# Kernel optimization log

Hardware: AMD Instinct MI355X
Metric: run time of the kernel (lower is better)

Reference implementation:

```python
import jax, jax.numpy as jnp
import numpy as np

B, T, D, K = 8, 2048, 384, 64

def setup_inputs() -> dict:
    key = jax.random.key(0)
    k1, k2, k3, k4 = jax.random.split(key, 4)
    x = jax.random.normal(k1, (B, T, D), dtype=jnp.float32)
    # torch nn.Linear default init scale ~ 1/sqrt(fan_in); use scaled normals
    Wq = jax.random.normal(k2, (D, K), dtype=jnp.float32) / np.sqrt(D)
    Wk = jax.random.normal(k3, (D, K), dtype=jnp.float32) / np.sqrt(D)
    Wv = jax.random.normal(k4, (D, D), dtype=jnp.float32) / np.sqrt(D)
    return {"x": x, "Wq": Wq, "Wk": Wk, "Wv": Wv}

def reference(x, Wq, Wk, Wv):
    # x: (B,T,D)
    q = jnp.einsum('btd,dk->btk', x, Wq)      # (B,T,K)
    k = jnp.einsum('btd,dk->btk', x, Wk)      # (B,T,K)
    v = jnp.einsum('btd,de->bte', x, Wv)      # (B,T,D)
    scores = jnp.einsum('bqk,bsk->bqs', q, k) / jnp.sqrt(jnp.float32(K))  # (B,T,T)
    causal = jnp.tril(jnp.ones((T, T), dtype=bool))
    scores = jnp.where(causal, scores, -jnp.inf)
    weights = jax.nn.softmax(scores, axis=-1)
    out = jnp.einsum('bqs,bse->bqe', weights, v)  # (B,T,D)
    return out
```

## Files before the change

### kernel.cpp

```cpp
#include <hip/hip_runtime.h>

#define TT 2048
#define DD 384

typedef float f32x4 __attribute__((ext_vector_type(4)));
typedef float f32x16 __attribute__((ext_vector_type(16)));
typedef short s16x8 __attribute__((ext_vector_type(8)));
typedef short s16x2 __attribute__((ext_vector_type(2)));
typedef unsigned int u32x4 __attribute__((ext_vector_type(4)));
typedef unsigned int u32x2 __attribute__((ext_vector_type(2)));

typedef __attribute__((address_space(3))) unsigned char* as3p;
typedef const __attribute__((address_space(1))) unsigned char* as1p;
#define GLLDS(gsrc, ldst) __builtin_amdgcn_global_load_lds((as1p)(gsrc), (as3p)(ldst), 16, 0, 0)

static __device__ __forceinline__ unsigned short f2bf(float f) {
    unsigned int u = __builtin_bit_cast(unsigned int, f);
    u = (u + 0x7fffu + ((u >> 16) & 1u)) >> 16;
    return (unsigned short)u;
}
static __device__ __forceinline__ unsigned int pk2(float a, float b) {
#if __has_builtin(__builtin_amdgcn_cvt_pk_bf16_f32)
    s16x2 t = __builtin_amdgcn_cvt_pk_bf16_f32(a, b);
    return __builtin_bit_cast(unsigned int, t);
#else
    unsigned int ua = __builtin_bit_cast(unsigned int, a);
    unsigned int ub = __builtin_bit_cast(unsigned int, b);
    ua = (ua + 0x7fffu + ((ua >> 16) & 1u)) >> 16;
    ub = (ub + 0x7fffu + ((ub >> 16) & 1u)) & 0xffff0000u;
    return ua | ub;
#endif
}

__global__ __launch_bounds__(256, 2) void qkv_gemm(
    const float* __restrict__ x, const float* __restrict__ Wq,
    const float* __restrict__ Wk, const float* __restrict__ Wv,
    unsigned short* __restrict__ qo, unsigned short* __restrict__ ko,
    unsigned short* __restrict__ vto)
{
    __shared__ __align__(16) unsigned short lds[16384];
    const int tid = threadIdx.x;
    const int l   = tid & 63;
    const int w   = tid >> 6;
    const int si  = l & 15;
    const int qq  = l >> 4;
    const int m0  = blockIdx.x * 128;
    const int nb  = blockIdx.y;
    const int wr  = w >> 1, wc = w & 1;

    const int bn = tid & 127;
    const int bk = (tid >> 7) * 16;
    const float* wsrc; int ldw;
    if (nb == 0) { wsrc = (bn < 64) ? (Wq + bn) : (Wk + (bn - 64)); ldw = 64; }
    else         { wsrc = Wv + (nb - 1) * 128 + bn;                 ldw = 384; }

    f32x4 acc[4][4];
    #pragma unroll
    for (int rt = 0; rt < 4; ++rt)
        #pragma unroll
        for (int ct = 0; ct < 4; ++ct) acc[rt][ct] = (f32x4){0.f, 0.f, 0.f, 0.f};

    for (int kt = 0; kt < 12; ++kt) {
        const int k0 = kt * 32;
        #pragma unroll
        for (int i = 0; i < 2; ++i) {
            const int u = tid + 256 * i, r = u >> 2, c = u & 3;
            const float* xp = x + (size_t)(m0 + r) * DD + k0 + c * 8;
            f32x4 x0 = *(const f32x4*)xp;
            f32x4 x1 = *(const f32x4*)(xp + 4);
            u32x4 av = (u32x4){pk2(x0[0], x0[1]), pk2(x0[2], x0[3]),
                               pk2(x1[0], x1[1]), pk2(x1[2], x1[3])};
            *(s16x8*)&lds[r * 32 + ((c ^ (r & 3)) * 8)] = __builtin_bit_cast(s16x8, av);
        }
        {
            float t[16];
            #pragma unroll
            for (int j = 0; j < 16; ++j) t[j] = wsrc[(size_t)(k0 + bk + j) * ldw];
            #pragma unroll
            for (int jj = 0; jj < 2; ++jj) {
                u32x4 bv = (u32x4){pk2(t[jj * 8 + 0], t[jj * 8 + 1]), pk2(t[jj * 8 + 2], t[jj * 8 + 3]),
                                   pk2(t[jj * 8 + 4], t[jj * 8 + 5]), pk2(t[jj * 8 + 6], t[jj * 8 + 7])};
                const int ch = (tid >> 7) * 2 + jj;
                *(s16x8*)&lds[4096 + bn * 32 + ((ch ^ (bn & 3)) * 8)] = __builtin_bit_cast(s16x8, bv);
            }
        }
        __syncthreads();

        s16x8 af[4], bf[4];
        #pragma unroll
        for (int rt = 0; rt < 4; ++rt) {
            const int row = wr * 64 + rt * 16 + si;
            af[rt] = *(const s16x8*)&lds[row * 32 + ((qq ^ (row & 3)) * 8)];
        }
        #pragma unroll
        for (int ct = 0; ct < 4; ++ct) {
            const int col = wc * 64 + ct * 16 + si;
            bf[ct] = *(const s16x8*)&lds[4096 + col * 32 + ((qq ^ (col & 3)) * 8)];
        }
        #pragma unroll
        for (int rt = 0; rt < 4; ++rt)
            #pragma unroll
            for (int ct = 0; ct < 4; ++ct)
                acc[rt][ct] = __builtin_amdgcn_mfma_f32_16x16x32_bf16(af[rt], bf[ct], acc[rt][ct], 0, 0, 0);
        __syncthreads();
    }

    if (nb == 0) {
        if (wc == 0) {
            #pragma unroll
            for (int rt = 0; rt < 4; ++rt)
                #pragma unroll
                for (int ct = 0; ct < 4; ++ct)
                    #pragma unroll
                    for (int r = 0; r < 4; ++r) {
                        const int m = m0 + wr * 64 + rt * 16 + qq * 4 + r;
                        qo[(size_t)m * 64 + ct * 16 + si] = f2bf(acc[rt][ct][r] * 0.125f);
                    }
        } else {
            #pragma unroll
            for (int rt = 0; rt < 4; ++rt)
                #pragma unroll
                for (int ct = 0; ct < 4; ++ct)
                    #pragma unroll
                    for (int r = 0; r < 4; ++r) {
                        const int m = m0 + wr * 64 + rt * 16 + qq * 4 + r;
                        const int col = ct * 16 + si;
                        ko[(size_t)m * 64 + (((col >> 3) ^ (m & 7)) * 8) + (col & 7)] = f2bf(acc[rt][ct][r]);
                    }
        }
    } else {
        #pragma unroll
        for (int rt = 0; rt < 4; ++rt)
            #pragma unroll
            for (int ct = 0; ct < 4; ++ct)
                #pragma unroll
                for (int r = 0; r < 4; ++r) {
                    const int m = wr * 64 + rt * 16 + qq * 4 + r;
                    const int n = wc * 64 + ct * 16 + si;
                    lds[n * 128 + (((m >> 3) ^ (n & 7)) * 8) + (m & 7)] = f2bf(acc[rt][ct][r]);
                }
        __syncthreads();
        const int bbat = m0 >> 11, t0 = m0 & 2047;
        #pragma unroll
        for (int i = 0; i < 8; ++i) {
            const int u = tid + 256 * i, n = u >> 4, mc = u & 15;
            s16x8 v = *(const s16x8*)&lds[n * 128 + ((mc ^ (n & 7)) * 8)];
            *(s16x8*)&vto[((size_t)bbat * DD + ((nb - 1) * 128 + n)) * TT
                          + t0 + (mc >> 3) * 64 + (((mc & 7) ^ (n & 7)) * 8)] = v;
        }
    }
}

__global__ __launch_bounds__(768, 3) void attn(
    const unsigned short* __restrict__ qg, const unsigned short* __restrict__ kg,
    const unsigned short* __restrict__ vg, float* __restrict__ out)
{
    __shared__ __align__(16) unsigned short lds[53248];

    const int tid = threadIdx.x;
    const int l   = tid & 63;
    const int w   = tid >> 6;
    const int qh  = w & 1;
    const int eu  = w >> 1;
    const bool isprod = (w < 4);
    const int lo  = l & 31;
    const int hi  = l >> 5;

    const int g  = blockIdx.x;
    const int bb = g & 7;
    const int eh = (g >> 3) & 1;
    const int pr = g >> 4;
    const int e0 = eh * 192;

    const unsigned short* kbase = kg + (size_t)bb * TT * 64;
    const unsigned short* vbase = vg + ((size_t)bb * DD + e0) * TT;

    #define STAGE(IT, KB, VB)                                                              \
    {                                                                                      \
        if (isprod) {                                                                      \
            GLLDS(kbase + (size_t)(IT) * 4096 + (2 * w) * 512 + l * 8,                     \
                  &lds[(KB) * 4096 + (2 * w) * 512]);                                      \
            GLLDS(kbase + (size_t)(IT) * 4096 + (2 * w + 1) * 512 + l * 8,                 \
                  &lds[(KB) * 4096 + (2 * w + 1) * 512]);                                  \
        } else {                                                                           \
            _Pragma("unroll")                                                              \
            for (int c3 = 0; c3 < 3; ++c3) {                                               \
                const int rg = 3 * (w - 4) + c3;                                           \
                GLLDS(vbase + (size_t)(rg * 8 + (l >> 3)) * TT + (IT) * 64 + (l & 7) * 8,  \
                      &lds[8192 + (VB) * 12288 + rg * 512]);                               \
            }                                                                              \
        }                                                                                  \
    }

    #define PVSTEP(VB, PB)                                                                 \
    {                                                                                      \
        __builtin_amdgcn_s_setprio(1);                                                     \
        _Pragma("unroll")                                                                  \
        for (int ss = 0; ss < 2; ++ss) {                                                   \
            const int pbse = 45056 + (PB) * 4096 + (qh * 2 + ss) * 1024;                   \
            s16x8 a0 = *(const s16x8*)&lds[pbse + l * 8];                                  \
            s16x8 a1 = *(const s16x8*)&lds[pbse + 512 + l * 8];                            \
            const int el = eu * 32 + lo;                                                   \
            const int vbse = 8192 + (VB) * 12288 + el * 64;                                \
            s16x8 v0 = *(const s16x8*)&lds[vbse + (((ss * 4 + hi) ^ (el & 7)) * 8)];       \
            o = __builtin_amdgcn_mfma_f32_32x32x16_bf16(a0, v0, o, 0, 0, 0);               \
            s16x8 v1 = *(const s16x8*)&lds[vbse + (((ss * 4 + 2 + hi) ^ (el & 7)) * 8)];   \
            o = __builtin_amdgcn_mfma_f32_32x32x16_bf16(a1, v1, o, 0, 0, 0);               \
        }                                                                                  \
        __builtin_amdgcn_s_setprio(0);                                                     \
    }

    for (int hf = 0; hf < 2; ++hf) {
        const int q2 = hf ? pr : 31 - pr;
        const int q0 = q2 * 64;
        const int qrow = q0 + qh * 32 + lo;

        s16x8 qf[4];
        if (isprod) {
            const unsigned short* qp = qg + ((size_t)bb * TT + qrow) * 64;
            #pragma unroll
            for (int st = 0; st < 4; ++st) qf[st] = *(const s16x8*)(qp + st * 16 + hi * 8);
        }

        f32x16 o;
        #pragma unroll
        for (int r = 0; r < 16; ++r) o[r] = 0.f;
        float lp = 0.f;

        STAGE(0, 0, 0);

        int vi = 0, vn = 1;
        for (int it = 0; it <= q2; ++it) {
            const int kb = it & 1;
            __syncthreads();

            if (it < q2) STAGE(it + 1, 1 - kb, vn);

            if (isprod) {
                f32x16 sa;
                #pragma unroll
                for (int r = 0; r < 16; ++r) sa[r] = 0.f;
                __builtin_amdgcn_s_setprio(1);
                #pragma unroll
                for (int st = 0; st < 4; ++st) {
                    s16x8 kf = *(const s16x8*)&lds[kb * 4096 + (eu * 32 + lo) * 64 + (((st * 2 + hi) ^ (lo & 7)) * 8)];
                    sa = __builtin_amdgcn_mfma_f32_32x32x16_bf16(kf, qf[st], sa, 0, 0, 0);
                }
                __builtin_amdgcn_s_setprio(0);
                const bool mb = (it == q2);
                float pv[16];
                #pragma unroll
                for (int r = 0; r < 16; ++r) {
                    float e = __expf(sa[r]);
                    if (mb) {
                        const int srow = it * 64 + eu * 32 + (r & 3) + 8 * (r >> 2) + 4 * hi;
                        if (srow > qrow) e = 0.f;
                    }
                    pv[r] = e;
                    lp += e;
                }
                unsigned int d0 = pk2(pv[0], pv[1]),   d1 = pk2(pv[2], pv[3]);
                unsigned int d2 = pk2(pv[4], pv[5]),   d3 = pk2(pv[6], pv[7]);
                unsigned int d4 = pk2(pv[8], pv[9]),   d5 = pk2(pv[10], pv[11]);
                unsigned int d6 = pk2(pv[12], pv[13]), d7 = pk2(pv[14], pv[15]);
                u32x4 fa0, fa1;
#if __has_builtin(__builtin_amdgcn_permlane32_swap)
                {
                    u32x2 s02 = __builtin_bit_cast(u32x2, __builtin_amdgcn_permlane32_swap(d0, d2, false, false));
                    u32x2 s13 = __builtin_bit_cast(u32x2, __builtin_amdgcn_permlane32_swap(d1, d3, false, false));
                    u32x2 s46 = __builtin_bit_cast(u32x2, __builtin_amdgcn_permlane32_swap(d4, d6, false, false));
                    u32x2 s57 = __builtin_bit_cast(u32x2, __builtin_amdgcn_permlane32_swap(d5, d7, false, false));
                    fa0 = (u32x4){s02[0], s13[0], s02[1], s13[1]};
                    fa1 = (u32x4){s46[0], s57[0], s46[1], s57[1]};
                }
#else
                {
                    unsigned int sA0 = hi ? d0 : d2, sA1 = hi ? d1 : d3;
                    unsigned int rA0 = (unsigned int)__shfl_xor((int)sA0, 32);
                    unsigned int rA1 = (unsigned int)__shfl_xor((int)sA1, 32);
                    fa0 = hi ? (u32x4){rA0, rA1, d2, d3} : (u32x4){d0, d1, rA0, rA1};
                    unsigned int sB0 = hi ? d4 : d6, sB1 = hi ? d5 : d7;
                    unsigned int rB0 = (unsigned int)__shfl_xor((int)sB0, 32);
                    unsigned int rB1 = (unsigned int)__shfl_xor((int)sB1, 32);
                    fa1 = hi ? (u32x4){rB0, rB1, d6, d7} : (u32x4){d4, d5, rB0, rB1};
                }
#endif
                *(s16x8*)&lds[45056 + kb * 4096 + (qh * 2 + eu) * 1024 + l * 8]       = __builtin_bit_cast(s16x8, fa0);
                *(s16x8*)&lds[45056 + kb * 4096 + (qh * 2 + eu) * 1024 + 512 + l * 8] = __builtin_bit_cast(s16x8, fa1);
            }

            if (it > 0) {
                const int vp = (vi == 0) ? 2 : vi - 1;
                PVSTEP(vp, 1 - kb);
            }

            vi = vn; vn = (vn == 2) ? 0 : vn + 1;
        }
        __syncthreads();
        {
            const int vlast = (vi == 0) ? 2 : vi - 1;
            PVSTEP(vlast, q2 & 1);
        }
        if (isprod) {
            float lt = lp + __shfl_xor(lp, 32);
            if (hi == 0) ((float*)lds)[(qh * 2 + eu) * 32 + lo] = lt;
        }
        __syncthreads();

        {
            const float* stL = (const float*)lds;
            #pragma unroll
            for (int r = 0; r < 16; ++r) {
                const int rloc = (r & 3) + 8 * (r >> 2) + 4 * hi;
                const float linv = 1.f / (stL[(qh * 2) * 32 + rloc] + stL[(qh * 2 + 1) * 32 + rloc]);
                out[((size_t)bb * TT + q0 + qh * 32 + rloc) * DD + e0 + eu * 32 + lo]
                    = o[r] * linv;
            }
        }
        __syncthreads();
    }
    #undef STAGE
    #undef PVSTEP
}

extern "C" void kernel_launch(void* const* d_in, const int* in_sizes, int n_in,
                              void* d_out, int out_size, void* d_ws, size_t ws_size,
                              hipStream_t stream)
{
    const float* x  = (const float*)d_in[0];
    const float* Wq = (const float*)d_in[1];
    const float* Wk = (const float*)d_in[2];
    const float* Wv = (const float*)d_in[3];

    unsigned short* qws  = (unsigned short*)d_ws;
    unsigned short* kws  = (unsigned short*)((char*)d_ws + ((size_t)2 << 20));
    unsigned short* vtws = (unsigned short*)((char*)d_ws + ((size_t)4 << 20));

    qkv_gemm<<<dim3(128, 4), dim3(256), 0, stream>>>(x, Wq, Wk, Wv, qws, kws, vtws);
    attn<<<dim3(256), dim3(768), 0, stream>>>(qws, kws, vtws, (float*)d_out);
}
```

Before: 133.4 us.

## Restructure attention to per-32-row query blocks with full-width value tiles

The attention kernel now assigns one 32-row query tile to each block, with 2 producer waves computing QK^T/exp and 6 consumer waves each covering 64 value columns over the full 384 width. This replaces the old scheme of 64-row tiles split into two 192-wide column halves and processed as paired heavy/light halves. V fragments are register double-buffered, each K tile's exp is computed once for all value columns, and blocks launch in descending work order. The QKV GEMM loops over two column blocks per workgroup, halving its grid. In exchange, the attention grid has more blocks with fewer threads each and uses more LDS and registers per block.

```diff
diff --git a/kernel.cpp b/kernel.cpp
--- a/kernel.cpp
+++ b/kernel.cpp
@@ -45,282 +45,300 @@
     const int si  = l & 15;
     const int qq  = l >> 4;
     const int m0  = blockIdx.x * 128;
-    const int nb  = blockIdx.y;
+    const int nbp = blockIdx.y;
     const int wr  = w >> 1, wc = w & 1;
 
     const int bn = tid & 127;
     const int bk = (tid >> 7) * 16;
-    const float* wsrc; int ldw;
-    if (nb == 0) { wsrc = (bn < 64) ? (Wq + bn) : (Wk + (bn - 64)); ldw = 64; }
-    else         { wsrc = Wv + (nb - 1) * 128 + bn;                 ldw = 384; }
-
-    f32x4 acc[4][4];
-    #pragma unroll
-    for (int rt = 0; rt < 4; ++rt)
-        #pragma unroll
-        for (int ct = 0; ct < 4; ++ct) acc[rt][ct] = (f32x4){0.f, 0.f, 0.f, 0.f};
-
-    for (int kt = 0; kt < 12; ++kt) {
-        const int k0 = kt * 32;
-        #pragma unroll
-        for (int i = 0; i < 2; ++i) {
-            const int u = tid + 256 * i, r = u >> 2, c = u & 3;
-            const float* xp = x + (size_t)(m0 + r) * DD + k0 + c * 8;
-            f32x4 x0 = *(const f32x4*)xp;
-            f32x4 x1 = *(const f32x4*)(xp + 4);
-            u32x4 av = (u32x4){pk2(x0[0], x0[1]), pk2(x0[2], x0[3]),
-                               pk2(x1[0], x1[1]), pk2(x1[2], x1[3])};
-            *(s16x8*)&lds[r * 32 + ((c ^ (r & 3)) * 8)] = __builtin_bit_cast(s16x8, av);
-        }
-        {
-            float t[16];
-            #pragma unroll
-            for (int j = 0; j < 16; ++j) t[j] = wsrc[(size_t)(k0 + bk + j) * ldw];
-            #pragma unroll
-            for (int jj = 0; jj < 2; ++jj) {
-                u32x4 bv = (u32x4){pk2(t[jj * 8 + 0], t[jj * 8 + 1]), pk2(t[jj * 8 + 2], t[jj * 8 + 3]),
-                                   pk2(t[jj * 8 + 4], t[jj * 8 + 5]), pk2(t[jj * 8 + 6], t[jj * 8 + 7])};
-                const int ch = (tid >> 7) * 2 + jj;
-                *(s16x8*)&lds[4096 + bn * 32 + ((ch ^ (bn & 3)) * 8)] = __builtin_bit_cast(s16x8, bv);
-            }
-        }
-        __syncthreads();
-
-        s16x8 af[4], bf[4];
-        #pragma unroll
-        for (int rt = 0; rt < 4; ++rt) {
-            const int row = wr * 64 + rt * 16 + si;
-            af[rt] = *(const s16x8*)&lds[row * 32 + ((qq ^ (row & 3)) * 8)];
-        }
-        #pragma unroll
-        for (int ct = 0; ct < 4; ++ct) {
-            const int col = wc * 64 + ct * 16 + si;
-            bf[ct] = *(const s16x8*)&lds[4096 + col * 32 + ((qq ^ (col & 3)) * 8)];
-        }
+
+    for (int nbi = 0; nbi < 2; ++nbi) {
+        const int nb = nbp * 2 + nbi;
+        const float* wsrc; int ldw;
+        if (nb == 0) { wsrc = (bn < 64) ? (Wq + bn) : (Wk + (bn - 64)); ldw = 64; }
+        else         { wsrc = Wv + (nb - 1) * 128 + bn;                 ldw = 384; }
+
+        f32x4 acc[4][4];
         #pragma unroll
         for (int rt = 0; rt < 4; ++rt)
             #pragma unroll
-            for (int ct = 0; ct < 4; ++ct)
-                acc[rt][ct] = __builtin_amdgcn_mfma_f32_16x16x32_bf16(af[rt], bf[ct], acc[rt][ct], 0, 0, 0);
-        __syncthreads();
-    }
-
-    if (nb == 0) {
-        if (wc == 0) {
+            for (int ct = 0; ct < 4; ++ct) acc[rt][ct] = (f32x4){0.f, 0.f, 0.f, 0.f};
+
+        for (int kt = 0; kt < 12; ++kt) {
+            const int k0 = kt * 32;
+            #pragma unroll
+            for (int i = 0; i < 2; ++i) {
+                const int u = tid + 256 * i, r = u >> 2, c = u & 3;
+                const float* xp = x + (size_t)(m0 + r) * DD + k0 + c * 8;
+                f32x4 x0 = *(const f32x4*)xp;
+                f32x4 x1 = *(const f32x4*)(xp + 4);
+                u32x4 av = (u32x4){pk2(x0[0], x0[1]), pk2(x0[2], x0[3]),
+                                   pk2(x1[0], x1[1]), pk2(x1[2], x1[3])};
+                *(s16x8*)&lds[r * 32 + ((c ^ (r & 3)) * 8)] = __builtin_bit_cast(s16x8, av);
+            }
+            {
+                float t[16];
+                #pragma unroll
+                for (int j = 0; j < 16; ++j) t[j] = wsrc[(size_t)(k0 + bk + j) * ldw];
+                #pragma unroll
+                for (int jj = 0; jj < 2; ++jj) {
+                    u32x4 bv = (u32x4){pk2(t[jj * 8 + 0], t[jj * 8 + 1]), pk2(t[jj * 8 + 2], t[jj * 8 + 3]),
+                                       pk2(t[jj * 8 + 4], t[jj * 8 + 5]), pk2(t[jj * 8 + 6], t[jj * 8 + 7])};
+                    const int ch = (tid >> 7) * 2 + jj;
+                    *(s16x8*)&lds[4096 + bn * 32 + ((ch ^ (bn & 3)) * 8)] = __builtin_bit_cast(s16x8, bv);
+                }
+            }
+            __syncthreads();
+
+            s16x8 af[4], bf[4];
+            #pragma unroll
+            for (int rt = 0; rt < 4; ++rt) {
+                const int row = wr * 64 + rt * 16 + si;
+                af[rt] = *(const s16x8*)&lds[row * 32 + ((qq ^ (row & 3)) * 8)];
+            }
+            #pragma unroll
+            for (int ct = 0; ct < 4; ++ct) {
+                const int col = wc * 64 + ct * 16 + si;
+                bf[ct] = *(const s16x8*)&lds[4096 + col * 32 + ((qq ^ (col & 3)) * 8)];
+            }
+            #pragma unroll
+            for (int rt = 0; rt < 4; ++rt)
+                #pragma unroll
+                for (int ct = 0; ct < 4; ++ct)
+                    acc[rt][ct] = __builtin_amdgcn_mfma_f32_16x16x32_bf16(af[rt], bf[ct], acc[rt][ct], 0, 0, 0);
+            __syncthreads();
+        }
+
+        if (nb == 0) {
+            if (wc == 0) {
+                #pragma unroll
+                for (int rt = 0; rt < 4; ++rt)
+                    #pragma unroll
+                    for (int ct = 0; ct < 4; ++ct)
+                        #pragma unroll
+                        for (int r = 0; r < 4; ++r) {
+                            const int m = m0 + wr * 64 + rt * 16 + qq * 4 + r;
+                            qo[(size_t)m * 64 + ct * 16 + si] = f2bf(acc[rt][ct][r] * 0.125f);
+                        }
+            } else {
+                #pragma unroll
+                for (int rt = 0; rt < 4; ++rt)
+                    #pragma unroll
+                    for (int ct = 0; ct < 4; ++ct)
+                        #pragma unroll
+                        for (int r = 0; r < 4; ++r) {
+                            const int m = m0 + wr * 64 + rt * 16 + qq * 4 + r;
+                            const int col = ct * 16 + si;
+                            ko[(size_t)m * 64 + (((col >> 3) ^ (m & 7)) * 8) + (col & 7)] = f2bf(acc[rt][ct][r]);
+                        }
+            }
+        } else {
             #pragma unroll
             for (int rt = 0; rt < 4; ++rt)
                 #pragma unroll
                 for (int ct = 0; ct < 4; ++ct)
                     #pragma unroll
                     for (int r = 0; r < 4; ++r) {
-                        const int m = m0 + wr * 64 + rt * 16 + qq * 4 + r;
-                        qo[(size_t)m * 64 + ct * 16 + si] = f2bf(acc[rt][ct][r] * 0.125f);
+                        const int m = wr * 64 + rt * 16 + qq * 4 + r;
+                        const int n = wc * 64 + ct * 16 + si;
+                        lds[n * 128 + (((m >> 3) ^ (n & 7)) * 8) + (m & 7)] = f2bf(acc[rt][ct][r]);
                     }
-        } else {
-            #pragma unroll
-            for (int rt = 0; rt < 4; ++rt)
-                #pragma unroll
-                for (int ct = 0; ct < 4; ++ct)
-                    #pragma unroll
-                    for (int r = 0; r < 4; ++r) {
-                        const int m = m0 + wr * 64 + rt * 16 + qq * 4 + r;
-                        const int col = ct * 16 + si;
-                        ko[(size_t)m * 64 + (((col >> 3) ^ (m & 7)) * 8) + (col & 7)] = f2bf(acc[rt][ct][r]);
-                    }
+            __syncthreads();
+            const int bbat = m0 >> 11, t0 = m0 & 2047;
+            #pragma unroll
+            for (int i = 0; i < 8; ++i) {
+                const int u = tid + 256 * i, n = u >> 4, mc = u & 15;
+                s16x8 v = *(const s16x8*)&lds[n * 128 + ((mc ^ (n & 7)) * 8)];
+                *(s16x8*)&vto[((size_t)bbat * DD + ((nb - 1) * 128 + n)) * TT
+                              + t0 + (mc >> 3) * 64 + (((mc & 7) ^ (n & 7)) * 8)] = v;
+            }
         }
-    } else {
-        #pragma unroll
-        for (int rt = 0; rt < 4; ++rt)
-            #pragma unroll
-            for (int ct = 0; ct < 4; ++ct)
-                #pragma unroll
-                for (int r = 0; r < 4; ++r) {
-                    const int m = wr * 64 + rt * 16 + qq * 4 + r;
-                    const int n = wc * 64 + ct * 16 + si;
-                    lds[n * 128 + (((m >> 3) ^ (n & 7)) * 8) + (m & 7)] = f2bf(acc[rt][ct][r]);
-                }
         __syncthreads();
-        const int bbat = m0 >> 11, t0 = m0 & 2047;
-        #pragma unroll
-        for (int i = 0; i < 8; ++i) {
-            const int u = tid + 256 * i, n = u >> 4, mc = u & 15;
-            s16x8 v = *(const s16x8*)&lds[n * 128 + ((mc ^ (n & 7)) * 8)];
-            *(s16x8*)&vto[((size_t)bbat * DD + ((nb - 1) * 128 + n)) * TT
-                          + t0 + (mc >> 3) * 64 + (((mc & 7) ^ (n & 7)) * 8)] = v;
-        }
-    }
-}
-
-__global__ __launch_bounds__(768, 3) void attn(
+    }
+}
+
+__global__ __launch_bounds__(512, 2) void attn(
     const unsigned short* __restrict__ qg, const unsigned short* __restrict__ kg,
     const unsigned short* __restrict__ vg, float* __restrict__ out)
 {
-    __shared__ __align__(16) unsigned short lds[53248];
+    __shared__ __align__(16) unsigned short lds[61440];
 
     const int tid = threadIdx.x;
     const int l   = tid & 63;
     const int w   = tid >> 6;
-    const int qh  = w & 1;
-    const int eu  = w >> 1;
-    const bool isprod = (w < 4);
+    const bool isprod = (w < 2);
+    const int cw  = w - 2;
     const int lo  = l & 31;
     const int hi  = l >> 5;
 
     const int g  = blockIdx.x;
     const int bb = g & 7;
-    const int eh = (g >> 3) & 1;
-    const int pr = g >> 4;
-    const int e0 = eh * 192;
+    const int q1 = 63 - (g >> 3);
+    const int q0 = q1 * 32;
+    const int itm = q1 >> 1;
+    const int qrow = q0 + lo;
+
+    s16x8 qf[4];
+    if (isprod) {
+        const unsigned short* qp = qg + ((size_t)bb * TT + qrow) * 64;
+        #pragma unroll
+        for (int st = 0; st < 4; ++st) qf[st] = *(const s16x8*)(qp + st * 16 + hi * 8);
+    }
+
+    f32x16 o[2];
+    #pragma unroll
+    for (int et = 0; et < 2; ++et)
+        #pragma unroll
+        for (int r = 0; r < 16; ++r) o[et][r] = 0.f;
+    float lp = 0.f;
+    s16x8 vfA[8], vfB[8];
 
     const unsigned short* kbase = kg + (size_t)bb * TT * 64;
-    const unsigned short* vbase = vg + ((size_t)bb * DD + e0) * TT;
-
-    #define STAGE(IT, KB, VB)                                                              \
+    const unsigned short* vbase = vg + (size_t)bb * DD * TT;
+
+    #define STAGE(IT, BUF)                                                                 \
     {                                                                                      \
         if (isprod) {                                                                      \
-            GLLDS(kbase + (size_t)(IT) * 4096 + (2 * w) * 512 + l * 8,                     \
-                  &lds[(KB) * 4096 + (2 * w) * 512]);                                      \
-            GLLDS(kbase + (size_t)(IT) * 4096 + (2 * w + 1) * 512 + l * 8,                 \
-                  &lds[(KB) * 4096 + (2 * w + 1) * 512]);                                  \
+            _Pragma("unroll")                                                              \
+            for (int c = 0; c < 4; ++c) {                                                  \
+                const int ch = w * 4 + c;                                                  \
+                GLLDS(kbase + (size_t)(IT) * 4096 + ch * 512 + l * 8,                      \
+                      &lds[(BUF) * 4096 + ch * 512]);                                      \
+            }                                                                              \
         } else {                                                                           \
             _Pragma("unroll")                                                              \
-            for (int c3 = 0; c3 < 3; ++c3) {                                               \
-                const int rg = 3 * (w - 4) + c3;                                           \
+            for (int c = 0; c < 8; ++c) {                                                  \
+                const int rg = cw * 8 + c;                                                 \
                 GLLDS(vbase + (size_t)(rg * 8 + (l >> 3)) * TT + (IT) * 64 + (l & 7) * 8,  \
-                      &lds[8192 + (VB) * 12288 + rg * 512]);                               \
+                      &lds[8192 + (BUF) * 24576 + rg * 512]);                              \
             }                                                                              \
         }                                                                                  \
     }
 
-    #define PVSTEP(VB, PB)                                                                 \
+    #define LOADV(VF, VB)                                                                  \
+    {                                                                                      \
+        _Pragma("unroll")                                                                  \
+        for (int ss = 0; ss < 2; ++ss)                                                     \
+            _Pragma("unroll")                                                              \
+            for (int et = 0; et < 2; ++et) {                                               \
+                const int el = cw * 64 + et * 32 + lo;                                     \
+                const int vbse = 8192 + (VB) * 24576 + el * 64;                            \
+                VF[ss * 4 + et * 2 + 0] = *(const s16x8*)&lds[vbse + (((ss * 4 + hi) ^ (el & 7)) * 8)];     \
+                VF[ss * 4 + et * 2 + 1] = *(const s16x8*)&lds[vbse + (((ss * 4 + 2 + hi) ^ (el & 7)) * 8)]; \
+            }                                                                              \
+    }
+
+    #define PVC(VF, PB)                                                                    \
     {                                                                                      \
         __builtin_amdgcn_s_setprio(1);                                                     \
         _Pragma("unroll")                                                                  \
         for (int ss = 0; ss < 2; ++ss) {                                                   \
-            const int pbse = 45056 + (PB) * 4096 + (qh * 2 + ss) * 1024;                   \
+            const int pbse = 57344 + (PB) * 2048 + ss * 1024;                              \
             s16x8 a0 = *(const s16x8*)&lds[pbse + l * 8];                                  \
             s16x8 a1 = *(const s16x8*)&lds[pbse + 512 + l * 8];                            \
-            const int el = eu * 32 + lo;                                                   \
-            const int vbse = 8192 + (VB) * 12288 + el * 64;                                \
-            s16x8 v0 = *(const s16x8*)&lds[vbse + (((ss * 4 + hi) ^ (el & 7)) * 8)];       \
-            o = __builtin_amdgcn_mfma_f32_32x32x16_bf16(a0, v0, o, 0, 0, 0);               \
-            s16x8 v1 = *(const s16x8*)&lds[vbse + (((ss * 4 + 2 + hi) ^ (el & 7)) * 8)];   \
-            o = __builtin_amdgcn_mfma_f32_32x32x16_bf16(a1, v1, o, 0, 0, 0);               \
+            _Pragma("unroll")                                                              \
+            for (int et = 0; et < 2; ++et) {                                               \
+                o[et] = __builtin_amdgcn_mfma_f32_32x32x16_bf16(a0, VF[ss * 4 + et * 2 + 0], o[et], 0, 0, 0); \
+                o[et] = __builtin_amdgcn_mfma_f32_32x32x16_bf16(a1, VF[ss * 4 + et * 2 + 1], o[et], 0, 0, 0); \
+            }                                                                              \
         }                                                                                  \
         __builtin_amdgcn_s_setprio(0);                                                     \
     }
 
-    for (int hf = 0; hf < 2; ++hf) {
-        const int q2 = hf ? pr : 31 - pr;
-        const int q0 = q2 * 64;
-        const int qrow = q0 + qh * 32 + lo;
-
-        s16x8 qf[4];
+    STAGE(0, 0);
+
+    for (int it = 0; it <= itm; ++it) {
+        const int kb = it & 1;
+        __syncthreads();
+
+        if (it < itm) STAGE(it + 1, 1 - kb);
+
         if (isprod) {
-            const unsigned short* qp = qg + ((size_t)bb * TT + qrow) * 64;
-            #pragma unroll
-            for (int st = 0; st < 4; ++st) qf[st] = *(const s16x8*)(qp + st * 16 + hi * 8);
+            f32x16 sa;
+            #pragma unroll
+            for (int r = 0; r < 16; ++r) sa[r] = 0.f;
+            __builtin_amdgcn_s_setprio(1);
+            #pragma unroll
+            for (int st = 0; st < 4; ++st) {
+                s16x8 kf = *(const s16x8*)&lds[kb * 4096 + (w * 32 + lo) * 64 + (((st * 2 + hi) ^ (lo & 7)) * 8)];
+                sa = __builtin_amdgcn_mfma_f32_32x32x16_bf16(kf, qf[st], sa, 0, 0, 0);
+            }
+            __builtin_amdgcn_s_setprio(0);
+            const bool mb = (it == itm);
+            float pv[16];
+            #pragma unroll
+            for (int r = 0; r < 16; ++r) {
+                float e = __expf(sa[r]);
+                if (mb) {
+                    const int srow = it * 64 + w * 32 + (r & 3) + 8 * (r >> 2) + 4 * hi;
+                    if (srow > qrow) e = 0.f;
+                }
+                pv[r] = e;
+                lp += e;
+            }
+            unsigned int d0 = pk2(pv[0], pv[1]),   d1 = pk2(pv[2], pv[3]);
+            unsigned int d2 = pk2(pv[4], pv[5]),   d3 = pk2(pv[6], pv[7]);
+            unsigned int d4 = pk2(pv[8], pv[9]),   d5 = pk2(pv[10], pv[11]);
+            unsigned int d6 = pk2(pv[12], pv[13]), d7 = pk2(pv[14], pv[15]);
+            u32x4 fa0, fa1;
+#if __has_builtin(__builtin_amdgcn_permlane32_swap)
+            {
+                u32x2 s02 = __builtin_bit_cast(u32x2, __builtin_amdgcn_permlane32_swap(d0, d2, false, false));
+                u32x2 s13 = __builtin_bit_cast(u32x2, __builtin_amdgcn_permlane32_swap(d1, d3, false, false));
+                u32x2 s46 = __builtin_bit_cast(u32x2, __builtin_amdgcn_permlane32_swap(d4, d6, false, false));
+                u32x2 s57 = __builtin_bit_cast(u32x2, __builtin_amdgcn_permlane32_swap(d5, d7, false, false));
+                fa0 = (u32x4){s02[0], s13[0], s02[1], s13[1]};
+                fa1 = (u32x4){s46[0], s57[0], s46[1], s57[1]};
+            }
+#else
+            {
+                unsigned int sA0 = hi ? d0 : d2, sA1 = hi ? d1 : d3;
+                unsigned int rA0 = (unsigned int)__shfl_xor((int)sA0, 32);
+                unsigned int rA1 = (unsigned int)__shfl_xor((int)sA1, 32);
+                fa0 = hi ? (u32x4){rA0, rA1, d2, d3} : (u32x4){d0, d1, rA0, rA1};
+                unsigned int sB0 = hi ? d4 : d6, sB1 = hi ? d5 : d7;
+                unsigned int rB0 = (unsigned int)__shfl_xor((int)sB0, 32);
+                unsigned int rB1 = (unsigned int)__shfl_xor((int)sB1, 32);
+                fa1 = hi ? (u32x4){rB0, rB1, d6, d7} : (u32x4){d4, d5, rB0, rB1};
+            }
+#endif
+            *(s16x8*)&lds[57344 + kb * 2048 + w * 1024 + l * 8]       = __builtin_bit_cast(s16x8, fa0);
+            *(s16x8*)&lds[57344 + kb * 2048 + w * 1024 + 512 + l * 8] = __builtin_bit_cast(s16x8, fa1);
+        } else {
+            if (it & 1) {
+                if (it > 0) PVC(vfA, 1 - kb);
+                LOADV(vfB, kb);
+            } else {
+                if (it > 0) PVC(vfB, 1 - kb);
+                LOADV(vfA, kb);
+            }
         }
-
-        f32x16 o;
+    }
+    __syncthreads();
+
+    if (isprod) {
+        float lt = lp + __shfl_xor(lp, 32);
+        if (hi == 0) ((float*)lds)[w * 32 + lo] = lt;
+    } else {
+        if (itm & 1) { PVC(vfB, itm & 1); }
+        else         { PVC(vfA, itm & 1); }
+    }
+    __syncthreads();
+
+    if (!isprod) {
+        const float* stL = (const float*)lds;
         #pragma unroll
-        for (int r = 0; r < 16; ++r) o[r] = 0.f;
-        float lp = 0.f;
-
-        STAGE(0, 0, 0);
-
-        int vi = 0, vn = 1;
-        for (int it = 0; it <= q2; ++it) {
-            const int kb = it & 1;
-            __syncthreads();
-
-            if (it < q2) STAGE(it + 1, 1 - kb, vn);
-
-            if (isprod) {
-                f32x16 sa;
-                #pragma unroll
-                for (int r = 0; r < 16; ++r) sa[r] = 0.f;
-                __builtin_amdgcn_s_setprio(1);
-                #pragma unroll
-                for (int st = 0; st < 4; ++st) {
-                    s16x8 kf = *(const s16x8*)&lds[kb * 4096 + (eu * 32 + lo) * 64 + (((st * 2 + hi) ^ (lo & 7)) * 8)];
-                    sa = __builtin_amdgcn_mfma_f32_32x32x16_bf16(kf, qf[st], sa, 0, 0, 0);
-                }
-                __builtin_amdgcn_s_setprio(0);
-                const bool mb = (it == q2);
-                float pv[16];
-                #pragma unroll
-                for (int r = 0; r < 16; ++r) {
-                    float e = __expf(sa[r]);
-                    if (mb) {
-                        const int srow = it * 64 + eu * 32 + (r & 3) + 8 * (r >> 2) + 4 * hi;
-                        if (srow > qrow) e = 0.f;
-                    }
-                    pv[r] = e;
-                    lp += e;
-                }
-                unsigned int d0 = pk2(pv[0], pv[1]),   d1 = pk2(pv[2], pv[3]);
-                unsigned int d2 = pk2(pv[4], pv[5]),   d3 = pk2(pv[6], pv[7]);
-                unsigned int d4 = pk2(pv[8], pv[9]),   d5 = pk2(pv[10], pv[11]);
-                unsigned int d6 = pk2(pv[12], pv[13]), d7 = pk2(pv[14], pv[15]);
-                u32x4 fa0, fa1;
-#if __has_builtin(__builtin_amdgcn_permlane32_swap)
-                {
-                    u32x2 s02 = __builtin_bit_cast(u32x2, __builtin_amdgcn_permlane32_swap(d0, d2, false, false));
-                    u32x2 s13 = __builtin_bit_cast(u32x2, __builtin_amdgcn_permlane32_swap(d1, d3, false, false));
-                    u32x2 s46 = __builtin_bit_cast(u32x2, __builtin_amdgcn_permlane32_swap(d4, d6, false, false));
-                    u32x2 s57 = __builtin_bit_cast(u32x2, __builtin_amdgcn_permlane32_swap(d5, d7, false, false));
-                    fa0 = (u32x4){s02[0], s13[0], s02[1], s13[1]};
-                    fa1 = (u32x4){s46[0], s57[0], s46[1], s57[1]};
-                }
-#else
-                {
-                    unsigned int sA0 = hi ? d0 : d2, sA1 = hi ? d1 : d3;
-                    unsigned int rA0 = (unsigned int)__shfl_xor((int)sA0, 32);
-                    unsigned int rA1 = (unsigned int)__shfl_xor((int)sA1, 32);
-                    fa0 = hi ? (u32x4){rA0, rA1, d2, d3} : (u32x4){d0, d1, rA0, rA1};
-                    unsigned int sB0 = hi ? d4 : d6, sB1 = hi ? d5 : d7;
-                    unsigned int rB0 = (unsigned int)__shfl_xor((int)sB0, 32);
-                    unsigned int rB1 = (unsigned int)__shfl_xor((int)sB1, 32);
-                    fa1 = hi ? (u32x4){rB0, rB1, d6, d7} : (u32x4){d4, d5, rB0, rB1};
-                }
-#endif
-                *(s16x8*)&lds[45056 + kb * 4096 + (qh * 2 + eu) * 1024 + l * 8]       = __builtin_bit_cast(s16x8, fa0);
-                *(s16x8*)&lds[45056 + kb * 4096 + (qh * 2 + eu) * 1024 + 512 + l * 8] = __builtin_bit_cast(s16x8, fa1);
-            }
-
-            if (it > 0) {
-                const int vp = (vi == 0) ? 2 : vi - 1;
-                PVSTEP(vp, 1 - kb);
-            }
-
-            vi = vn; vn = (vn == 2) ? 0 : vn + 1;
-        }
-        __syncthreads();
-        {
-            const int vlast = (vi == 0) ? 2 : vi - 1;
-            PVSTEP(vlast, q2 & 1);
-        }
-        if (isprod) {
-            float lt = lp + __shfl_xor(lp, 32);
-            if (hi == 0) ((float*)lds)[(qh * 2 + eu) * 32 + lo] = lt;
-        }
-        __syncthreads();
-
-        {
-            const float* stL = (const float*)lds;
+        for (int et = 0; et < 2; ++et)
             #pragma unroll
             for (int r = 0; r < 16; ++r) {
                 const int rloc = (r & 3) + 8 * (r >> 2) + 4 * hi;
-                const float linv = 1.f / (stL[(qh * 2) * 32 + rloc] + stL[(qh * 2 + 1) * 32 + rloc]);
-                out[((size_t)bb * TT + q0 + qh * 32 + rloc) * DD + e0 + eu * 32 + lo]
-                    = o[r] * linv;
-            }
-        }
-        __syncthreads();
+                const float linv = 1.f / (stL[rloc] + stL[32 + rloc]);
+                out[((size_t)bb * TT + q0 + rloc) * DD + cw * 64 + et * 32 + lo]
+                    = o[et][r] * linv;
+            }
     }
     #undef STAGE
-    #undef PVSTEP
+    #undef LOADV
+    #undef PVC
 }
 
 extern "C" void kernel_launch(void* const* d_in, const int* in_sizes, int n_in,
@@ -336,6 +354,6 @@
     unsigned short* kws  = (unsigned short*)((char*)d_ws + ((size_t)2 << 20));
     unsigned short* vtws = (unsigned short*)((char*)d_ws + ((size_t)4 << 20));
 
-    qkv_gemm<<<dim3(128, 4), dim3(256), 0, stream>>>(x, Wq, Wk, Wv, qws, kws, vtws);
-    attn<<<dim3(256), dim3(768), 0, stream>>>(qws, kws, vtws, (float*)d_out);
-}
+    qkv_gemm<<<dim3(128, 2), dim3(256), 0, stream>>>(x, Wq, Wk, Wv, qws, kws, vtws);
+    attn<<<dim3(512), dim3(512), 0, stream>>>(qws, kws, vtws, (float*)d_out);
+}
```

Result: slower. 176.6 us (+32.4%).

## Pre-pack weights to bf16 and double-buffer QKV GEMM with direct LDS loads

Applied to the files above, without the earlier changes.

A new small kernel converts Wq, Wk and Wv each call into one packed, pre-swizzled bf16 weight matrix in workspace. The QKV GEMM then streams weight tiles straight into LDS with global_load_lds and double-buffers the x and W stages, so the next tile loads while MFMAs run. The M tile is halved to 64 rows, which doubles the grid and raises the occupancy hint, and the V-transpose epilogue is simplified to match. The cost is an extra kernel launch and more workspace traffic in exchange for removing strided fp32 weight loads and conversions from the GEMM inner loop.

```diff
diff --git a/kernel.cpp b/kernel.cpp
--- a/kernel.cpp
+++ b/kernel.cpp
@@ -32,121 +32,140 @@
 #endif
 }
 
-__global__ __launch_bounds__(256, 2) void qkv_gemm(
-    const float* __restrict__ x, const float* __restrict__ Wq,
-    const float* __restrict__ Wk, const float* __restrict__ Wv,
+__global__ __launch_bounds__(256, 8) void wprep(
+    const float* __restrict__ Wq, const float* __restrict__ Wk, const float* __restrict__ Wv,
+    unsigned short* __restrict__ wall)
+{
+    const int gid = blockIdx.x * 256 + threadIdx.x;
+    const int col = gid & 511;
+    const int kt  = gid >> 9;
+    unsigned short* op = wall + (size_t)col * 384 + kt * 32;
+    #pragma unroll
+    for (int c = 0; c < 4; ++c) {
+        u32x4 v;
+        #pragma unroll
+        for (int j2 = 0; j2 < 4; ++j2) {
+            const int k = kt * 32 + c * 8 + j2 * 2;
+            float f0 = (col < 64)  ? Wq[(size_t)k * 64 + col]
+                     : (col < 128) ? Wk[(size_t)k * 64 + (col - 64)]
+                                   : Wv[(size_t)k * 384 + (col - 128)];
+            float f1 = (col < 64)  ? Wq[(size_t)(k + 1) * 64 + col]
+                     : (col < 128) ? Wk[(size_t)(k + 1) * 64 + (col - 64)]
+                                   : Wv[(size_t)(k + 1) * 384 + (col - 128)];
+            v[j2] = pk2(f0, f1);
+        }
+        *(s16x8*)(op + ((c ^ (col & 3)) * 8)) = __builtin_bit_cast(s16x8, v);
+    }
+}
+
+__global__ __launch_bounds__(256, 4) void qkv_gemm(
+    const float* __restrict__ x, const unsigned short* __restrict__ wall,
     unsigned short* __restrict__ qo, unsigned short* __restrict__ ko,
     unsigned short* __restrict__ vto)
 {
-    __shared__ __align__(16) unsigned short lds[16384];
+    __shared__ __align__(16) unsigned short lds[12288];
     const int tid = threadIdx.x;
     const int l   = tid & 63;
     const int w   = tid >> 6;
     const int si  = l & 15;
     const int qq  = l >> 4;
-    const int m0  = blockIdx.x * 128;
+    const int m0  = blockIdx.x * 64;
     const int nb  = blockIdx.y;
     const int wr  = w >> 1, wc = w & 1;
 
-    const int bn = tid & 127;
-    const int bk = (tid >> 7) * 16;
-    const float* wsrc; int ldw;
-    if (nb == 0) { wsrc = (bn < 64) ? (Wq + bn) : (Wk + (bn - 64)); ldw = 64; }
-    else         { wsrc = Wv + (nb - 1) * 128 + bn;                 ldw = 384; }
-
-    f32x4 acc[4][4];
+    const int ar = tid >> 2, ac = tid & 3;
+    const float* xs = x + (size_t)(m0 + ar) * DD + ac * 8;
+    const unsigned short* ws = wall + (size_t)nb * 128 * 384;
+
+#define QSTAGE(KT, B)                                                                      \
+    {                                                                                      \
+        _Pragma("unroll")                                                                  \
+        for (int c2 = 0; c2 < 2; ++c2) {                                                   \
+            const int ch = w * 2 + c2;                                                     \
+            GLLDS(ws + (size_t)(ch * 16 + (l >> 2)) * 384 + (KT) * 32 + (l & 3) * 8,       \
+                  &lds[(B) * 6144 + 2048 + ch * 512]);                                     \
+        }                                                                                  \
+        f32x4 x0 = *(const f32x4*)(xs + (KT) * 32);                                        \
+        f32x4 x1 = *(const f32x4*)(xs + (KT) * 32 + 4);                                    \
+        u32x4 av = (u32x4){pk2(x0[0], x0[1]), pk2(x0[2], x0[3]),                           \
+                           pk2(x1[0], x1[1]), pk2(x1[2], x1[3])};                          \
+        *(s16x8*)&lds[(B) * 6144 + ar * 32 + ((ac ^ (ar & 3)) * 8)] =                      \
+            __builtin_bit_cast(s16x8, av);                                                 \
+    }
+
+    f32x4 acc[2][4];
     #pragma unroll
-    for (int rt = 0; rt < 4; ++rt)
+    for (int rt = 0; rt < 2; ++rt)
         #pragma unroll
         for (int ct = 0; ct < 4; ++ct) acc[rt][ct] = (f32x4){0.f, 0.f, 0.f, 0.f};
 
+    QSTAGE(0, 0);
     for (int kt = 0; kt < 12; ++kt) {
-        const int k0 = kt * 32;
-        #pragma unroll
-        for (int i = 0; i < 2; ++i) {
-            const int u = tid + 256 * i, r = u >> 2, c = u & 3;
-            const float* xp = x + (size_t)(m0 + r) * DD + k0 + c * 8;
-            f32x4 x0 = *(const f32x4*)xp;
-            f32x4 x1 = *(const f32x4*)(xp + 4);
-            u32x4 av = (u32x4){pk2(x0[0], x0[1]), pk2(x0[2], x0[3]),
-                               pk2(x1[0], x1[1]), pk2(x1[2], x1[3])};
-            *(s16x8*)&lds[r * 32 + ((c ^ (r & 3)) * 8)] = __builtin_bit_cast(s16x8, av);
-        }
-        {
-            float t[16];
-            #pragma unroll
-            for (int j = 0; j < 16; ++j) t[j] = wsrc[(size_t)(k0 + bk + j) * ldw];
-            #pragma unroll
-            for (int jj = 0; jj < 2; ++jj) {
-                u32x4 bv = (u32x4){pk2(t[jj * 8 + 0], t[jj * 8 + 1]), pk2(t[jj * 8 + 2], t[jj * 8 + 3]),
-                                   pk2(t[jj * 8 + 4], t[jj * 8 + 5]), pk2(t[jj * 8 + 6], t[jj * 8 + 7])};
-                const int ch = (tid >> 7) * 2 + jj;
-                *(s16x8*)&lds[4096 + bn * 32 + ((ch ^ (bn & 3)) * 8)] = __builtin_bit_cast(s16x8, bv);
-            }
-        }
-        __syncthreads();
-
-        s16x8 af[4], bf[4];
-        #pragma unroll
-        for (int rt = 0; rt < 4; ++rt) {
-            const int row = wr * 64 + rt * 16 + si;
-            af[rt] = *(const s16x8*)&lds[row * 32 + ((qq ^ (row & 3)) * 8)];
+        const int b = kt & 1;
+        __syncthreads();
+        if (kt < 11) QSTAGE(kt + 1, 1 - b);
+
+        s16x8 af[2], bf[4];
+        #pragma unroll
+        for (int rt = 0; rt < 2; ++rt) {
+            const int row = wr * 32 + rt * 16 + si;
+            af[rt] = *(const s16x8*)&lds[b * 6144 + row * 32 + ((qq ^ (row & 3)) * 8)];
         }
         #pragma unroll
         for (int ct = 0; ct < 4; ++ct) {
             const int col = wc * 64 + ct * 16 + si;
-            bf[ct] = *(const s16x8*)&lds[4096 + col * 32 + ((qq ^ (col & 3)) * 8)];
-        }
-        #pragma unroll
-        for (int rt = 0; rt < 4; ++rt)
+            bf[ct] = *(const s16x8*)&lds[b * 6144 + 2048 + col * 32 + ((qq ^ (col & 3)) * 8)];
+        }
+        #pragma unroll
+        for (int rt = 0; rt < 2; ++rt)
             #pragma unroll
             for (int ct = 0; ct < 4; ++ct)
                 acc[rt][ct] = __builtin_amdgcn_mfma_f32_16x16x32_bf16(af[rt], bf[ct], acc[rt][ct], 0, 0, 0);
-        __syncthreads();
-    }
+    }
+    __syncthreads();
+#undef QSTAGE
 
     if (nb == 0) {
         if (wc == 0) {
             #pragma unroll
-            for (int rt = 0; rt < 4; ++rt)
+            for (int rt = 0; rt < 2; ++rt)
                 #pragma unroll
                 for (int ct = 0; ct < 4; ++ct)
                     #pragma unroll
                     for (int r = 0; r < 4; ++r) {
-                        const int m = m0 + wr * 64 + rt * 16 + qq * 4 + r;
+                        const int m = m0 + wr * 32 + rt * 16 + qq * 4 + r;
                         qo[(size_t)m * 64 + ct * 16 + si] = f2bf(acc[rt][ct][r] * 0.125f);
                     }
         } else {
             #pragma unroll
-            for (int rt = 0; rt < 4; ++rt)
+            for (int rt = 0; rt < 2; ++rt)
                 #pragma unroll
                 for (int ct = 0; ct < 4; ++ct)
                     #pragma unroll
                     for (int r = 0; r < 4; ++r) {
-                        const int m = m0 + wr * 64 + rt * 16 + qq * 4 + r;
+                        const int m = m0 + wr * 32 + rt * 16 + qq * 4 + r;
                         const int col = ct * 16 + si;
                         ko[(size_t)m * 64 + (((col >> 3) ^ (m & 7)) * 8) + (col & 7)] = f2bf(acc[rt][ct][r]);
                     }
         }
     } else {
         #pragma unroll
-        for (int rt = 0; rt < 4; ++rt)
+        for (int rt = 0; rt < 2; ++rt)
             #pragma unroll
             for (int ct = 0; ct < 4; ++ct)
                 #pragma unroll
                 for (int r = 0; r < 4; ++r) {
-                    const int m = wr * 64 + rt * 16 + qq * 4 + r;
+                    const int m = wr * 32 + rt * 16 + qq * 4 + r;
                     const int n = wc * 64 + ct * 16 + si;
-                    lds[n * 128 + (((m >> 3) ^ (n & 7)) * 8) + (m & 7)] = f2bf(acc[rt][ct][r]);
+                    lds[n * 64 + (((m >> 3) ^ (n & 7)) * 8) + (m & 7)] = f2bf(acc[rt][ct][r]);
                 }
         __syncthreads();
         const int bbat = m0 >> 11, t0 = m0 & 2047;
         #pragma unroll
-        for (int i = 0; i < 8; ++i) {
-            const int u = tid + 256 * i, n = u >> 4, mc = u & 15;
-            s16x8 v = *(const s16x8*)&lds[n * 128 + ((mc ^ (n & 7)) * 8)];
-            *(s16x8*)&vto[((size_t)bbat * DD + ((nb - 1) * 128 + n)) * TT
-                          + t0 + (mc >> 3) * 64 + (((mc & 7) ^ (n & 7)) * 8)] = v;
+        for (int i = 0; i < 4; ++i) {
+            const int u = tid + 256 * i, n = u >> 3, p = u & 7;
+            *(s16x8*)&vto[((size_t)bbat * DD + ((nb - 1) * 128 + n)) * TT + t0 + p * 8]
+                = *(const s16x8*)&lds[n * 64 + p * 8];
         }
     }
 }
@@ -335,7 +354,9 @@
     unsigned short* qws  = (unsigned short*)d_ws;
     unsigned short* kws  = (unsigned short*)((char*)d_ws + ((size_t)2 << 20));
     unsigned short* vtws = (unsigned short*)((char*)d_ws + ((size_t)4 << 20));
-
-    qkv_gemm<<<dim3(128, 4), dim3(256), 0, stream>>>(x, Wq, Wk, Wv, qws, kws, vtws);
+    unsigned short* wall = (unsigned short*)((char*)d_ws + ((size_t)16 << 20));
+
+    wprep<<<dim3(24), dim3(256), 0, stream>>>(Wq, Wk, Wv, wall);
+    qkv_gemm<<<dim3(256, 4), dim3(256), 0, stream>>>(x, wall, qws, kws, vtws);
     attn<<<dim3(256), dim3(768), 0, stream>>>(qws, kws, vtws, (float*)d_out);
 }
```

Measured after the change: 128.5 us. -3.6%, faster.
